# Kernel tuning notes

Hardware: AMD Instinct MI355X
Metric: run time of the kernel (lower is better)

Reference implementation:

```python
import jax, jax.numpy as jnp
import numpy as np

DIM = 1024
N_HEADS = 16
D_K = DIM // N_HEADS
B, N = 2, 2048


def _pairwise_dist(p):
    # p: [B, N, 3] -> Euclidean cdist [B, N, N], grad-safe at zero distance
    sq = jnp.sum(p * p, axis=-1)                      # [B, N]
    d2 = sq[:, :, None] + sq[:, None, :] - 2.0 * jnp.einsum('bnd,bmd->bnm', p, p)
    d2 = jnp.maximum(d2, 0.0)
    safe = jnp.where(d2 > 0.0, d2, 1.0)
    return jnp.where(d2 > 0.0, jnp.sqrt(safe), 0.0)


def setup_inputs() -> dict:
    key = jax.random.key(0)
    ks = jax.random.split(key, 11)
    s = 1.0 / np.sqrt(DIM)
    inp = {
        'x': jax.random.normal(ks[0], (B, N, DIM), jnp.float32),
        'positions': jax.random.normal(ks[1], (B, N, 3), jnp.float32),
        'W_q': jax.random.normal(ks[2], (DIM, DIM), jnp.float32) * s,
        'b_q': jnp.zeros((DIM,), jnp.float32),
        'W_k': jax.random.normal(ks[3], (DIM, DIM), jnp.float32) * s,
        'b_k': jnp.zeros((DIM,), jnp.float32),
        'W_v': jax.random.normal(ks[4], (DIM, DIM), jnp.float32) * s,
        'b_v': jnp.zeros((DIM,), jnp.float32),
        'W_o': jax.random.normal(ks[5], (DIM, DIM), jnp.float32) * s,
        'b_o': jnp.zeros((DIM,), jnp.float32),
        'dist_bias': jax.random.normal(ks[6], (N_HEADS, 1, 1), jnp.float32),
    }
    return inp


def reference(x, positions, W_q, b_q, W_k, b_k, W_v, b_v, W_o, b_o, dist_bias):
    Bv, Nv, C = x.shape
    def proj(W, b):
        # [B,N,C] -> [B,H,N,d_k]
        return (x @ W.T + b).reshape(Bv, Nv, N_HEADS, D_K).transpose(0, 2, 1, 3)
    Q = proj(W_q, b_q)
    K = proj(W_k, b_k)
    V = proj(W_v, b_v)
    attn = jnp.einsum('bhnd,bhmd->bhnm', Q, K) / np.sqrt(D_K)  # [B,H,N,N]
    dists = _pairwise_dist(positions)                          # [B,N,N]
    # log(exp(-|b|*d) + 1e-8), per-head bias broadcast over [B,H,N,N]
    dist_weights = jnp.exp(-jnp.abs(dist_bias)[None] * dists[:, None])
    attn = attn + jnp.log(dist_weights + 1e-8)
    attn = jax.nn.softmax(attn, axis=-1)
    out = jnp.einsum('bhnm,bhmd->bhnd', attn, V)               # [B,H,N,d_k]
    out = out.transpose(0, 2, 1, 3).reshape(Bv, Nv, C)
    return out @ W_o.T + b_o
```

## Files before the change

### kernel.cpp

```cpp
#include <hip/hip_runtime.h>
#include <hip/hip_bf16.h>
#include <stdint.h>

using bf16   = __hip_bfloat16;
using short8 = __attribute__((ext_vector_type(8))) short;
using f32x4  = __attribute__((ext_vector_type(4))) float;
using f32x16 = __attribute__((ext_vector_type(16))) float;

#define NSEQ   2048
#define NHEADS 16
#define DK     64
#define DMODEL 1024
#define LOG2E  1.44269504088896f

#define GLDS16(gp, lp) __builtin_amdgcn_global_load_lds( \
    (const __attribute__((address_space(1))) void*)(gp), \
    (__attribute__((address_space(3))) void*)(lp), 16, 0, 0)

__device__ __forceinline__ ushort f2bf(float f){
  bf16 h = __float2bfloat16(f);
  return __builtin_bit_cast(ushort, h);
}
__device__ __forceinline__ float bf2f(ushort u){
  uint t = ((uint)u)<<16; return __builtin_bit_cast(float, t);
}

__global__ void k_cvt_geo(const float4* __restrict__ x,  const float4* __restrict__ wq,
                          const float4* __restrict__ wk, const float4* __restrict__ wv,
                          const float4* __restrict__ wo,
                          ushort4* __restrict__ xb,  ushort4* __restrict__ wqb,
                          ushort4* __restrict__ wkb, ushort4* __restrict__ wvb,
                          ushort4* __restrict__ wob,
                          const float* __restrict__ pos,
                          ushort* __restrict__ AF, ushort* __restrict__ BF){
  if (blockIdx.x >= 10240){
    const int i = (blockIdx.x - 10240)*blockDim.x + threadIdx.x;
    if (i >= 2*NSEQ) return;
    float px = pos[i*3+0], py = pos[i*3+1], pz = pos[i*3+2];
    float sq = px*px + py*py + pz*pz;
    ushort xh = f2bf(px); float xhf = bf2f(xh); ushort xl = f2bf(px - xhf);
    ushort yh = f2bf(py); float yhf = bf2f(yh); ushort yl = f2bf(py - yhf);
    ushort zh = f2bf(pz); float zhf = bf2f(zh); ushort zl = f2bf(pz - zhf);
    ushort sh = f2bf(sq); float shf = bf2f(sh); ushort sl = f2bf(sq - shf);
    ushort m2xh = f2bf(-2.f*xhf), m2xl = f2bf(-2.f*bf2f(xl));
    ushort m2yh = f2bf(-2.f*yhf), m2yl = f2bf(-2.f*bf2f(yl));
    ushort m2zh = f2bf(-2.f*zhf), m2zl = f2bf(-2.f*bf2f(zl));
    const ushort one = 0x3F80;
    ushort af[16] = {xh,xl,xh, yh,yl,yh, zh,zl,zh, sh,sl, one,one, 0,0,0};
    ushort bv[16] = {m2xh,m2xh,m2xl, m2yh,m2yh,m2yl, m2zh,m2zh,m2zl, one,one, sh,sl, 0,0,0};
    *(uint4*)&AF[i*16]     = *(uint4*)&af[0];
    *(uint4*)&AF[i*16 + 8] = *(uint4*)&af[8];
    *(uint4*)&BF[i*16]     = *(uint4*)&bv[0];
    *(uint4*)&BF[i*16 + 8] = *(uint4*)&bv[8];
    return;
  }
  const int i = blockIdx.x*blockDim.x + threadIdx.x;
  const float4* s; ushort4* d; int off;
  if (i < 1048576){ s = x; d = xb; off = i; }
  else {
    const int wi = i - 1048576;
    const int w  = wi >> 18;
    off = wi & 262143;
    switch(w){
      case 0:  s = wq; d = wqb; break;
      case 1:  s = wk; d = wkb; break;
      case 2:  s = wv; d = wvb; break;
      default: s = wo; d = wob; break;
    }
  }
  float4 v = s[off];
  ushort4 o;
  o.x = f2bf(v.x); o.y = f2bf(v.y); o.z = f2bf(v.z); o.w = f2bf(v.w);
  d[off] = o;
}

__device__ __forceinline__ void gemm_core(
    const ushort* __restrict__ Ap, const ushort* __restrict__ Bp,
    int bm, int bn, int tid, ushort smem[2][2][4096], f32x4 (&acc)[4][4])
{
  const int wave = tid>>6, lane = tid&63;
  const int wr = wave>>1, wc = wave&1;
  const int ko   = (lane>>4)*8;
  const int srow = wave*16 + (lane>>2);
  const int scol = (lane&3)*8;

  const ushort* As = Ap + (size_t)(bm*128)*DMODEL + scol;
  const ushort* Bs = Bp + (size_t)(bn*128)*DMODEL + scol;

#define STAGEG(buf, kt) do { \
    _Pragma("unroll") \
    for (int i_=0;i_<2;i_++){ \
      GLDS16(As + (size_t)(i_*64 + srow)*DMODEL + (kt)*32, &smem[buf][0][i_*2048 + wave*512]); \
      GLDS16(Bs + (size_t)(i_*64 + srow)*DMODEL + (kt)*32, &smem[buf][1][i_*2048 + wave*512]); \
    } } while(0)

  STAGEG(0, 0);
  for (int kt=0; kt<32; ++kt){
    int cur = kt&1;
    __syncthreads();
    if (kt<31) STAGEG(cur^1, kt+1);
    short8 af[4], bfv[4];
    const ushort* At = smem[cur][0];
    const ushort* Bt = smem[cur][1];
    #pragma unroll
    for (int mi=0;mi<4;mi++) af[mi]  = *(const short8*)&At[(wr*64+mi*16+(lane&15))*32 + ko];
    #pragma unroll
    for (int ni=0;ni<4;ni++) bfv[ni] = *(const short8*)&Bt[(wc*64+ni*16+(lane&15))*32 + ko];
    #pragma unroll
    for (int mi=0;mi<4;mi++)
      #pragma unroll
      for (int ni=0;ni<4;ni++)
        acc[mi][ni] = __builtin_amdgcn_mfma_f32_16x16x32_bf16(af[mi], bfv[ni], acc[mi][ni], 0,0,0);
  }
#undef STAGEG
}

__global__ __launch_bounds__(256) void k_gemm_qkv(
    const ushort* __restrict__ xb,
    const ushort* __restrict__ Wqb, const ushort* __restrict__ Wkb, const ushort* __restrict__ Wvb,
    const float* __restrict__ bq, const float* __restrict__ bk, const float* __restrict__ bv,
    ushort* __restrict__ Qo, ushort* __restrict__ Ko, ushort* __restrict__ Vto)
{
  __shared__ ushort smem[2][2][4096];
  const int tid = threadIdx.x;
  const int work = (blockIdx.x & 7)*96 + (blockIdx.x >> 3);
  const int t = work & 255;
  const int z = work >> 8;
  const int lane = tid&63, wave = tid>>6;
  const int wr = wave>>1, wc = wave&1;

  const ushort* Ap; const ushort* Bp; const float* bias;
  ushort* outp; int bm, bn; float scale = 1.0f;
  if (z==0){ Ap=xb;  Bp=Wqb; bias=bq; outp=Qo;  bm=t>>3; bn=t&7; scale=0.125f*LOG2E; }
  else if (z==1){ Ap=xb;  Bp=Wkb; bias=bk; outp=Ko;  bm=t>>3; bn=t&7; }
  else          { Ap=Wvb; Bp=xb;  bias=bv; outp=Vto; bm=t&7;  bn=t>>3; }

  f32x4 acc[4][4] = {};
  gemm_core(Ap, Bp, bm, bn, tid, smem, acc);

  if (z<2){
    #pragma unroll
    for (int mi=0;mi<4;mi++){
      const int m0 = bm*128 + wr*64 + mi*16 + (lane>>4)*4;
      #pragma unroll
      for (int ni=0;ni<4;ni++){
        const int nn = bn*128 + wc*64 + ni*16 + (lane&15);
        const float bs = bias[nn];
        const int h = nn>>6, d = nn&63;
        #pragma unroll
        for (int j=0;j<4;j++){
          int mm = m0+j;
          int b = mm>>11, nr = mm&2047;
          size_t off = (((size_t)(b*NHEADS+h)*NSEQ) + nr)*DK + d;
          outp[off] = f2bf((acc[mi][ni][j] + bs)*scale);
        }
      }
    }
  } else {
    #pragma unroll
    for (int mi=0;mi<4;mi++){
      const int m0 = bm*128 + wr*64 + mi*16 + (lane>>4)*4;
      #pragma unroll
      for (int ni=0;ni<4;ni++){
        const int nn = bn*128 + wc*64 + ni*16 + (lane&15);
        const int b = nn>>11, nr = nn&2047;
        #pragma unroll
        for (int j=0;j<4;j++){
          int mm = m0+j;
          const float bs = bias[mm];
          int h = mm>>6, d = mm&63;
          size_t off = (((size_t)(b*NHEADS+h)*DK) + d)*NSEQ + nr;
          outp[off] = f2bf(acc[mi][ni][j] + bs);
        }
      }
    }
  }
}

__global__ __launch_bounds__(256) void k_gemm_out(
    const ushort* __restrict__ Ob, const ushort* __restrict__ Wob,
    const float* __restrict__ bo, float* __restrict__ out)
{
  __shared__ ushort sa[2][4096];
  __shared__ ushort sb[2][2048];
  const int tid = threadIdx.x;
  const int work = (blockIdx.x & 7)*64 + (blockIdx.x >> 3);
  const int bm = work>>4, bn = work&15;
  const int lane = tid&63, wave = tid>>6;
  const int wr = wave>>1, wc = wave&1;
  const int ko   = (lane>>4)*8;
  const int srow = wave*16 + (lane>>2);
  const int scol = (lane&3)*8;

  const ushort* As = Ob  + (size_t)(bm*128)*DMODEL + scol;
  const ushort* Bs = Wob + (size_t)(bn*64)*DMODEL + scol;

#define STAGEO(buf, kt) do { \
    _Pragma("unroll") \
    for (int i_=0;i_<2;i_++) \
      GLDS16(As + (size_t)(i_*64 + srow)*DMODEL + (kt)*32, &sa[buf][i_*2048 + wave*512]); \
    GLDS16(Bs + (size_t)srow*DMODEL + (kt)*32, &sb[buf][wave*512]); \
  } while(0)

  f32x4 acc[4][2] = {};
  STAGEO(0, 0);
  for (int kt=0; kt<32; ++kt){
    int cur = kt&1;
    __syncthreads();
    if (kt<31) STAGEO(cur^1, kt+1);
    short8 af[4], bfv[2];
    #pragma unroll
    for (int mi=0;mi<4;mi++) af[mi]  = *(const short8*)&sa[cur][(wr*64+mi*16+(lane&15))*32 + ko];
    #pragma unroll
    for (int ni=0;ni<2;ni++) bfv[ni] = *(const short8*)&sb[cur][(wc*32+ni*16+(lane&15))*32 + ko];
    #pragma unroll
    for (int mi=0;mi<4;mi++)
      #pragma unroll
      for (int ni=0;ni<2;ni++)
        acc[mi][ni] = __builtin_amdgcn_mfma_f32_16x16x32_bf16(af[mi], bfv[ni], acc[mi][ni], 0,0,0);
  }
#undef STAGEO
  #pragma unroll
  for (int mi=0;mi<4;mi++){
    const int m0 = bm*128 + wr*64 + mi*16 + (lane>>4)*4;
    #pragma unroll
    for (int ni=0;ni<2;ni++){
      const int nn = bn*64 + wc*32 + ni*16 + (lane&15);
      const float bs = bo[nn];
      #pragma unroll
      for (int j=0;j<4;j++)
        out[(size_t)(m0+j)*DMODEL + nn] = acc[mi][ni][j] + bs;
    }
  }
}

__global__ __launch_bounds__(256) void k_attn(
    const ushort* __restrict__ Q, const ushort* __restrict__ K, const ushort* __restrict__ Vt,
    const ushort* __restrict__ AF, const ushort* __restrict__ BF,
    const float* __restrict__ dist_bias,
    ushort* __restrict__ O)
{
  __shared__ ushort kb[2][4096];
  __shared__ ushort vb[2][4096];
  __shared__ ushort ab[2][1024];
  const int tid = threadIdx.x, wave = tid>>6, lane = tid&63;
  const int qt = blockIdx.x, h = blockIdx.y, b = blockIdx.z;
  const int lo5 = lane&31, hi = lane>>5;
  const float ah2 = fabsf(dist_bias[h]) * LOG2E;
  const ushort* Qh  = Q  + ((size_t)(b*NHEADS+h))*NSEQ*DK;
  const ushort* Kh  = K  + ((size_t)(b*NHEADS+h))*NSEQ*DK;
  const ushort* Vth = Vt + ((size_t)(b*NHEADS+h))*DK*NSEQ;
  const ushort* AFb = AF + (size_t)b*NSEQ*16;
  const ushort* BFb = BF + (size_t)b*NSEQ*16;

  const int q0 = qt*128 + wave*32;

  short8 qf[4];
  #pragma unroll
  for (int s=0;s<4;s++)
    qf[s] = *(const short8*)&Qh[(size_t)(q0+lo5)*DK + s*16 + hi*8];
  const short8 bfq = *(const short8*)&BFb[(size_t)(q0+lo5)*16 + hi*8];

  const int grow  = lane>>3;
  const int gc16  = (lane&7) ^ grow;
  const int rowb  = wave*8 + grow;

#define STAGE(buf, jb) do { \
    _Pragma("unroll") \
    for (int p_=0;p_<2;p_++){ \
      const int rw_ = p_*32 + rowb; \
      GLDS16(Kh  + (size_t)((jb)+rw_)*DK   + gc16*8, &kb[buf][(p_*256 + wave*64)*8]); \
      GLDS16(Vth + (size_t)rw_*NSEQ + (jb) + gc16*8, &vb[buf][(p_*256 + wave*64)*8]); \
    } \
    if (wave < 2) \
      GLDS16(AFb + (size_t)((jb) + wave*32 + (lane>>1))*16 + (lane&1)*8, &ab[buf][wave*512]); \
  } while(0)

  const int rb = lo5*64;
  const int rx = lo5 & 7;

  f32x16 o0 = {}, o1 = {};
  float l_run = 0.f;

  STAGE(0, 0);
  for (int t=0; t<32; ++t){
    const int cur = t&1;
    __syncthreads();
    if (t<31) STAGE(cur^1, (t+1)*64);
    const ushort* kbc = kb[cur];
    const ushort* vbc = vb[cur];
    const ushort* abc = ab[cur];
    #pragma unroll
    for (int ss=0; ss<2; ++ss){
      const short8 afk = *(const short8*)&abc[(ss*32+lo5)*16 + hi*8];
      f32x16 zz = {};
      f32x16 d2 = __builtin_amdgcn_mfma_f32_32x32x16_bf16(afk, bfq, zz, 0,0,0);
      const short8 kf0 = *(const short8*)&kbc[ss*2048 + rb + (((0+hi)^rx)<<3)];
      const short8 kf1 = *(const short8*)&kbc[ss*2048 + rb + (((2+hi)^rx)<<3)];
      const short8 kf2 = *(const short8*)&kbc[ss*2048 + rb + (((4+hi)^rx)<<3)];
      const short8 kf3 = *(const short8*)&kbc[ss*2048 + rb + (((6+hi)^rx)<<3)];
      __builtin_amdgcn_s_setprio(1);
      f32x16 st = {};
      st = __builtin_amdgcn_mfma_f32_32x32x16_bf16(kf0, qf[0], st, 0,0,0);
      st = __builtin_amdgcn_mfma_f32_32x32x16_bf16(kf1, qf[1], st, 0,0,0);
      st = __builtin_amdgcn_mfma_f32_32x32x16_bf16(kf2, qf[2], st, 0,0,0);
      st = __builtin_amdgcn_mfma_f32_32x32x16_bf16(kf3, qf[3], st, 0,0,0);
      __builtin_amdgcn_s_setprio(0);
      float p[16];
      #pragma unroll
      for (int r=0;r<16;r++){
        float d = __builtin_amdgcn_sqrtf(fmaxf(d2[r], 0.f));
        p[r] = __builtin_exp2f(fmaf(-ah2, d, st[r]));
      }
      float s01=p[0]+p[1], s23=p[2]+p[3], s45=p[4]+p[5], s67=p[6]+p[7];
      float s89=p[8]+p[9], sab=p[10]+p[11], scd=p[12]+p[13], sef=p[14]+p[15];
      float rsum = ((s01+s23)+(s45+s67)) + ((s89+sab)+(scd+sef));
      rsum += __shfl_xor(rsum, 32);
      l_run += rsum;
      __builtin_amdgcn_s_setprio(1);
      #pragma unroll
      for (int s=0;s<2;s++){
        uint w0, w1, w2, w3;
        asm("v_cvt_pk_bf16_f32 %0, %1, %2" : "=v"(w0) : "v"(p[8*s+0]), "v"(p[8*s+1]));
        asm("v_cvt_pk_bf16_f32 %0, %1, %2" : "=v"(w2) : "v"(p[8*s+4]), "v"(p[8*s+5]));
        asm("v_cvt_pk_bf16_f32 %0, %1, %2" : "=v"(w1) : "v"(p[8*s+2]), "v"(p[8*s+3]));
        asm("v_cvt_pk_bf16_f32 %0, %1, %2" : "=v"(w3) : "v"(p[8*s+6]), "v"(p[8*s+7]));
        asm volatile("v_permlane32_swap_b32 %0, %1" : "+v"(w0), "+v"(w2));
        asm volatile("v_permlane32_swap_b32 %0, %1" : "+v"(w1), "+v"(w3));
        uint4 aw; aw.x = w0; aw.y = w1; aw.z = w2; aw.w = w3;
        const short8 pa = __builtin_bit_cast(short8, aw);
        const int jcol = (ss<<2) + 2*s + hi;
        const short8 v0 = *(const short8*)&vbc[       rb + ((jcol^rx)<<3)];
        const short8 v1 = *(const short8*)&vbc[2048 + rb + ((jcol^rx)<<3)];
        o0 = __builtin_amdgcn_mfma_f32_32x32x16_bf16(pa, v0, o0, 0,0,0);
        o1 = __builtin_amdgcn_mfma_f32_32x32x16_bf16(pa, v1, o1, 0,0,0);
      }
      __builtin_amdgcn_s_setprio(0);
    }
  }
#undef STAGE

  #pragma unroll
  for (int r=0;r<16;r++){
    const int src = (r&3) + 8*(r>>2) + 4*hi;
    const float lr = __shfl(l_run, src);
    const float inv = 1.f/lr;
    const int i = q0 + src;
    O[((size_t)b*NSEQ + i)*DMODEL + h*DK + lo5]      = f2bf(o0[r]*inv);
    O[((size_t)b*NSEQ + i)*DMODEL + h*DK + 32 + lo5] = f2bf(o1[r]*inv);
  }
}

extern "C" void kernel_launch(void* const* d_in, const int* in_sizes, int n_in,
                              void* d_out, int out_size, void* d_ws, size_t ws_size,
                              hipStream_t stream) {
  const float* x   = (const float*)d_in[0];
  const float* pos = (const float*)d_in[1];
  const float* Wq  = (const float*)d_in[2];
  const float* bq  = (const float*)d_in[3];
  const float* Wk  = (const float*)d_in[4];
  const float* bk  = (const float*)d_in[5];
  const float* Wv  = (const float*)d_in[6];
  const float* bv  = (const float*)d_in[7];
  const float* Wo  = (const float*)d_in[8];
  const float* bo  = (const float*)d_in[9];
  const float* db  = (const float*)d_in[10];
  float* out = (float*)d_out;

  char* ws = (char*)d_ws;
  ushort* xb   = (ushort*)(ws);
  ushort* Wqb  = (ushort*)(ws + ((size_t)8<<20));
  ushort* Wkb  = (ushort*)(ws + ((size_t)10<<20));
  ushort* Wvb  = (ushort*)(ws + ((size_t)12<<20));
  ushort* Wob  = (ushort*)(ws + ((size_t)14<<20));
  ushort* Qb   = (ushort*)(ws + ((size_t)16<<20));
  ushort* Kb   = (ushort*)(ws + ((size_t)24<<20));
  ushort* Vtb  = (ushort*)(ws + ((size_t)32<<20));
  ushort* AFt  = (ushort*)(ws + ((size_t)40<<20));
  ushort* BFt  = (ushort*)(ws + ((size_t)40<<20) + (128<<10));
  ushort* Omrg = xb;

  k_cvt_geo<<<10256, 256, 0, stream>>>(
      (const float4*)x, (const float4*)Wq, (const float4*)Wk, (const float4*)Wv, (const float4*)Wo,
      (ushort4*)xb, (ushort4*)Wqb, (ushort4*)Wkb, (ushort4*)Wvb, (ushort4*)Wob,
      pos, AFt, BFt);
  k_gemm_qkv<<<768, 256, 0, stream>>>(xb, Wqb, Wkb, Wvb, bq, bk, bv, Qb, Kb, Vtb);
  k_attn<<<dim3(16,NHEADS,2), 256, 0, stream>>>(Qb, Kb, Vtb, AFt, BFt, db, Omrg);
  k_gemm_out<<<512, 256, 0, stream>>>(Omrg, Wob, bo, out);
}
```

Baseline: 247.1 us.

## Split MFMA accumulator chains and load distance factors directly from global

Measured after the change: 254.5 us. 1.03x slower.

```diff
diff --git a/kernel.cpp b/kernel.cpp
--- a/kernel.cpp
+++ b/kernel.cpp
@@ -242,7 +242,6 @@
 {
   __shared__ ushort kb[2][4096];
   __shared__ ushort vb[2][4096];
-  __shared__ ushort ab[2][1024];
   const int tid = threadIdx.x, wave = tid>>6, lane = tid&63;
   const int qt = blockIdx.x, h = blockIdx.y, b = blockIdx.z;
   const int lo5 = lane&31, hi = lane>>5;
@@ -271,15 +270,12 @@
       const int rw_ = p_*32 + rowb; \
       GLDS16(Kh  + (size_t)((jb)+rw_)*DK   + gc16*8, &kb[buf][(p_*256 + wave*64)*8]); \
       GLDS16(Vth + (size_t)rw_*NSEQ + (jb) + gc16*8, &vb[buf][(p_*256 + wave*64)*8]); \
-    } \
-    if (wave < 2) \
-      GLDS16(AFb + (size_t)((jb) + wave*32 + (lane>>1))*16 + (lane&1)*8, &ab[buf][wave*512]); \
-  } while(0)
+    } } while(0)
 
   const int rb = lo5*64;
   const int rx = lo5 & 7;
 
-  f32x16 o0 = {}, o1 = {};
+  f32x16 o0a = {}, o0b = {}, o1a = {}, o1b = {};
   float l_run = 0.f;
 
   STAGE(0, 0);
@@ -289,35 +285,32 @@
     if (t<31) STAGE(cur^1, (t+1)*64);
     const ushort* kbc = kb[cur];
     const ushort* vbc = vb[cur];
-    const ushort* abc = ab[cur];
     #pragma unroll
     for (int ss=0; ss<2; ++ss){
-      const short8 afk = *(const short8*)&abc[(ss*32+lo5)*16 + hi*8];
+      const int jb = t*64 + ss*32;
+      const short8 afk = *(const short8*)&AFb[(size_t)(jb+lo5)*16 + hi*8];
       f32x16 zz = {};
       f32x16 d2 = __builtin_amdgcn_mfma_f32_32x32x16_bf16(afk, bfq, zz, 0,0,0);
       const short8 kf0 = *(const short8*)&kbc[ss*2048 + rb + (((0+hi)^rx)<<3)];
       const short8 kf1 = *(const short8*)&kbc[ss*2048 + rb + (((2+hi)^rx)<<3)];
       const short8 kf2 = *(const short8*)&kbc[ss*2048 + rb + (((4+hi)^rx)<<3)];
       const short8 kf3 = *(const short8*)&kbc[ss*2048 + rb + (((6+hi)^rx)<<3)];
-      __builtin_amdgcn_s_setprio(1);
-      f32x16 st = {};
-      st = __builtin_amdgcn_mfma_f32_32x32x16_bf16(kf0, qf[0], st, 0,0,0);
-      st = __builtin_amdgcn_mfma_f32_32x32x16_bf16(kf1, qf[1], st, 0,0,0);
-      st = __builtin_amdgcn_mfma_f32_32x32x16_bf16(kf2, qf[2], st, 0,0,0);
-      st = __builtin_amdgcn_mfma_f32_32x32x16_bf16(kf3, qf[3], st, 0,0,0);
-      __builtin_amdgcn_s_setprio(0);
+      f32x16 stA = {}, stB = {};
+      stA = __builtin_amdgcn_mfma_f32_32x32x16_bf16(kf0, qf[0], stA, 0,0,0);
+      stB = __builtin_amdgcn_mfma_f32_32x32x16_bf16(kf2, qf[2], stB, 0,0,0);
+      stA = __builtin_amdgcn_mfma_f32_32x32x16_bf16(kf1, qf[1], stA, 0,0,0);
+      stB = __builtin_amdgcn_mfma_f32_32x32x16_bf16(kf3, qf[3], stB, 0,0,0);
       float p[16];
       #pragma unroll
       for (int r=0;r<16;r++){
         float d = __builtin_amdgcn_sqrtf(fmaxf(d2[r], 0.f));
-        p[r] = __builtin_exp2f(fmaf(-ah2, d, st[r]));
+        p[r] = __builtin_exp2f(fmaf(-ah2, d, stA[r] + stB[r]));
       }
       float s01=p[0]+p[1], s23=p[2]+p[3], s45=p[4]+p[5], s67=p[6]+p[7];
       float s89=p[8]+p[9], sab=p[10]+p[11], scd=p[12]+p[13], sef=p[14]+p[15];
       float rsum = ((s01+s23)+(s45+s67)) + ((s89+sab)+(scd+sef));
       rsum += __shfl_xor(rsum, 32);
       l_run += rsum;
-      __builtin_amdgcn_s_setprio(1);
       #pragma unroll
       for (int s=0;s<2;s++){
         uint w0, w1, w2, w3;
@@ -332,10 +325,14 @@
         const int jcol = (ss<<2) + 2*s + hi;
         const short8 v0 = *(const short8*)&vbc[       rb + ((jcol^rx)<<3)];
         const short8 v1 = *(const short8*)&vbc[2048 + rb + ((jcol^rx)<<3)];
-        o0 = __builtin_amdgcn_mfma_f32_32x32x16_bf16(pa, v0, o0, 0,0,0);
-        o1 = __builtin_amdgcn_mfma_f32_32x32x16_bf16(pa, v1, o1, 0,0,0);
+        if (s==0){
+          o0a = __builtin_amdgcn_mfma_f32_32x32x16_bf16(pa, v0, o0a, 0,0,0);
+          o1a = __builtin_amdgcn_mfma_f32_32x32x16_bf16(pa, v1, o1a, 0,0,0);
+        } else {
+          o0b = __builtin_amdgcn_mfma_f32_32x32x16_bf16(pa, v0, o0b, 0,0,0);
+          o1b = __builtin_amdgcn_mfma_f32_32x32x16_bf16(pa, v1, o1b, 0,0,0);
+        }
       }
-      __builtin_amdgcn_s_setprio(0);
     }
   }
 #undef STAGE
@@ -346,8 +343,8 @@
     const float lr = __shfl(l_run, src);
     const float inv = 1.f/lr;
     const int i = q0 + src;
-    O[((size_t)b*NSEQ + i)*DMODEL + h*DK + lo5]      = f2bf(o0[r]*inv);
-    O[((size_t)b*NSEQ + i)*DMODEL + h*DK + 32 + lo5] = f2bf(o1[r]*inv);
+    O[((size_t)b*NSEQ + i)*DMODEL + h*DK + lo5]      = f2bf((o0a[r]+o0b[r])*inv);
+    O[((size_t)b*NSEQ + i)*DMODEL + h*DK + 32 + lo5] = f2bf((o1a[r]+o1b[r])*inv);
   }
 }
 
```
